# Kernel tuning notes

Measured on AMD Instinct MI355X. Metric: run time of the kernel, lower is better.

Reference implementation:

```python
import jax, jax.numpy as jnp
import numpy as np

B, S, D = 4, 4096, 1024
H = 16
HD = D // H  # 64
EPS = 1e-6


def setup_inputs() -> dict:
    key = jax.random.key(0)
    ks = jax.random.split(key, 7)
    scale = 1.0 / np.sqrt(D)
    return {
        "hidden_states": jax.random.normal(ks[0], (B, S, D), dtype=jnp.float32),
        "Wq": jax.random.normal(ks[1], (D, D), dtype=jnp.float32) * scale,
        "bq": jax.random.normal(ks[2], (D,), dtype=jnp.float32) * 0.02,
        "Wk": jax.random.normal(ks[3], (D, D), dtype=jnp.float32) * scale,
        "bk": jax.random.normal(ks[4], (D,), dtype=jnp.float32) * 0.02,
        "Wv": jax.random.normal(ks[5], (D, D), dtype=jnp.float32) * scale,
        "bv": jax.random.normal(ks[6], (D,), dtype=jnp.float32) * 0.02,
    }


def _heads(x):
    # [B,S,D] -> [B,H,S,HD]
    return x.reshape(B, S, H, HD).transpose(0, 2, 1, 3)


def reference(hidden_states, Wq, bq, Wk, bk, Wv, bv):
    q = _heads(hidden_states @ Wq + bq)
    k = _heads(hidden_states @ Wk + bk)
    v = _heads(hidden_states @ Wv + bv)
    # elu+1 feature maps
    q_feat = jax.nn.elu(q) + 1.0
    k_feat = jax.nn.elu(k) + 1.0
    # kv: [B,H,HD,HD]; k_sum: [B,H,HD]
    kv = jnp.einsum("bhsd,bhse->bhde", k_feat, v)
    k_sum = k_feat.sum(axis=2)
    numerator = jnp.einsum("bhsd,bhde->bhse", q_feat, kv)
    denominator = jnp.einsum("bhsd,bhd->bhs", q_feat, k_sum)
    denominator = jnp.maximum(denominator, EPS)
    out = numerator / denominator[..., None]  # [B,H,S,HD]
    return out.transpose(0, 2, 1, 3).reshape(B, S, D)
```

## Files before the change

kernel.cpp:

```cpp
#include <hip/hip_runtime.h>
#include <math.h>

#define BB 4
#define SS 4096
#define DD 1024
#define HH 16
#define HDD 64
#define MM (BB*SS)
#define EPSV 1e-6f

typedef __bf16 bf16x8 __attribute__((ext_vector_type(8)));
typedef float  f32x4  __attribute__((ext_vector_type(4)));
typedef unsigned short ushort_t;

__device__ __forceinline__ float bf2f(unsigned int u16) {
    return __uint_as_float(u16 << 16);
}
__device__ __forceinline__ unsigned short f2bf(float f) {
    unsigned int x = __float_as_uint(f);
    unsigned int r = x + 0x7fffu + ((x >> 16) & 1u);
    return (unsigned short)(r >> 16);
}

#define GLDS16(g, l) __builtin_amdgcn_global_load_lds( \
    (const __attribute__((address_space(1))) void*)(g), \
    (__attribute__((address_space(3))) void*)(l), 16, 0, 0)

__global__ __launch_bounds__(256) void cvt_hs(const float* __restrict__ in,
                                              ushort_t* __restrict__ out) {
    size_t i = ((size_t)blockIdx.x * 256 + threadIdx.x) * 8;
    float4 f0 = *reinterpret_cast<const float4*>(&in[i]);
    float4 f1 = *reinterpret_cast<const float4*>(&in[i + 4]);
    uint4 u;
    u.x = (unsigned)f2bf(f0.x) | ((unsigned)f2bf(f0.y) << 16);
    u.y = (unsigned)f2bf(f0.z) | ((unsigned)f2bf(f0.w) << 16);
    u.z = (unsigned)f2bf(f1.x) | ((unsigned)f2bf(f1.y) << 16);
    u.w = (unsigned)f2bf(f1.z) | ((unsigned)f2bf(f1.w) << 16);
    *reinterpret_cast<uint4*>(&out[i]) = u;
}

__global__ __launch_bounds__(256) void cvt_w(const float* __restrict__ Wq,
                                             const float* __restrict__ Wk,
                                             const float* __restrict__ Wv,
                                             ushort_t* __restrict__ wt) {
    const int z = blockIdx.z;
    const float* __restrict__ W = (z == 0) ? Wq : (z == 1) ? Wk : Wv;
    const int k0 = blockIdx.x * 64;
    const int n0 = blockIdx.y * 64;
    __shared__ float tile[64][65];
    const int t = threadIdx.x;
    {
        const int kk = t >> 2;
        const int c0 = (t & 3) * 16;
#pragma unroll
        for (int c = 0; c < 4; c++) {
            float4 v = *reinterpret_cast<const float4*>(&W[(size_t)(k0 + kk) * DD + n0 + c0 + c * 4]);
            tile[kk][c0 + c * 4 + 0] = v.x;
            tile[kk][c0 + c * 4 + 1] = v.y;
            tile[kk][c0 + c * 4 + 2] = v.z;
            tile[kk][c0 + c * 4 + 3] = v.w;
        }
    }
    __syncthreads();
    const int n = t >> 2;
    const int kc = t & 3;
    unsigned short tmp[16];
#pragma unroll
    for (int jj = 0; jj < 16; jj++) tmp[jj] = f2bf(tile[kc * 16 + jj][n]);
    uint4 u0, u1;
    u0.x = tmp[0] | (tmp[1] << 16);  u0.y = tmp[2] | (tmp[3] << 16);
    u0.z = tmp[4] | (tmp[5] << 16);  u0.w = tmp[6] | (tmp[7] << 16);
    u1.x = tmp[8] | (tmp[9] << 16);  u1.y = tmp[10] | (tmp[11] << 16);
    u1.z = tmp[12] | (tmp[13] << 16); u1.w = tmp[14] | (tmp[15] << 16);
    ushort_t* dst = &wt[((size_t)z << 20) + (size_t)(n0 + n) * DD + k0 + kc * 16];
    *reinterpret_cast<uint4*>(dst) = u0;
    *reinterpret_cast<uint4*>(dst + 8) = u1;
}

__global__ __launch_bounds__(256) void qkv_gemm_bf16(
    const ushort_t* __restrict__ A,
    const ushort_t* __restrict__ Bt,
    const float* __restrict__ bq, const float* __restrict__ bk, const float* __restrict__ bv,
    ushort_t* __restrict__ qf, ushort_t* __restrict__ kt, ushort_t* __restrict__ vt)
{
    const int id  = blockIdx.x;
    const int swz = (id & 7) * 384 + (id >> 3);
    const int z   = swz >> 10;
    const int rem = swz & 1023;
    const int m0  = (rem >> 3) * 128;
    const int n0  = (rem & 7) * 128;

    const ushort_t* __restrict__ Bz = Bt + ((size_t)z << 20);
    const float* __restrict__ bias  = (z == 0) ? bq : (z == 1) ? bk : bv;

    __shared__ ushort_t As[128 * 32];
    __shared__ ushort_t Bs[128 * 32];

    const int tid = threadIdx.x;
    const int lane = tid & 63;
    const int w  = tid >> 6;
    const int wr = w >> 1;
    const int wc = w & 1;

    f32x4 acc[4][4];
#pragma unroll
    for (int i = 0; i < 4; i++)
#pragma unroll
        for (int j = 0; j < 4; j++) acc[i][j] = (f32x4){0.f, 0.f, 0.f, 0.f};

    const int lrow = lane >> 2;
    const int lkc  = (lane & 3) * 8;
    const int fr = lane & 15;
    const int fk = (lane >> 4) * 8;

    for (int k0 = 0; k0 < DD; k0 += 32) {
        __syncthreads();
#pragma unroll
        for (int si = 0; si < 2; si++) {
            const int seg = w * 2 + si;
            GLDS16(&A [(size_t)(m0 + seg * 16 + lrow) * DD + k0 + lkc], &As[seg * 512]);
            GLDS16(&Bz[(size_t)(n0 + seg * 16 + lrow) * DD + k0 + lkc], &Bs[seg * 512]);
        }
        __syncthreads();
        bf16x8 a[4], b[4];
#pragma unroll
        for (int i = 0; i < 4; i++)
            a[i] = *reinterpret_cast<const bf16x8*>(&As[(wr * 64 + i * 16 + fr) * 32 + fk]);
#pragma unroll
        for (int j = 0; j < 4; j++)
            b[j] = *reinterpret_cast<const bf16x8*>(&Bs[(wc * 64 + j * 16 + fr) * 32 + fk]);
#pragma unroll
        for (int i = 0; i < 4; i++)
#pragma unroll
            for (int j = 0; j < 4; j++)
                acc[i][j] = __builtin_amdgcn_mfma_f32_16x16x32_bf16(a[i], b[j], acc[i][j], 0, 0, 0);
    }

    const int fq = lane >> 4;
    float bias4[4];
#pragma unroll
    for (int j = 0; j < 4; j++) bias4[j] = bias[n0 + wc * 64 + j * 16 + fr];

    if (z == 0) {
#pragma unroll
        for (int i = 0; i < 4; i++) {
#pragma unroll
            for (int r = 0; r < 4; r++) {
                const int m = m0 + wr * 64 + i * 16 + fq * 4 + r;
                const int bI = m >> 12;
                const int s  = m & 4095;
#pragma unroll
                for (int j = 0; j < 4; j++) {
                    const int n = n0 + wc * 64 + j * 16 + fr;
                    const int h = n >> 6, e = n & 63;
                    float c = acc[i][j][r] + bias4[j];
                    c = (c > 0.f) ? (c + 1.f) : __expf(c);
                    qf[((size_t)(bI * HH + h) * SS + s) * HDD + e] = f2bf(c);
                }
            }
        }
    } else {
        ushort_t* __restrict__ outt = (z == 1) ? kt : vt;
        const bool isk = (z == 1);
#pragma unroll
        for (int i = 0; i < 4; i++) {
            const int m = m0 + wr * 64 + i * 16 + fq * 4;
            const int bI = m >> 12;
            const int s  = m & 4095;
#pragma unroll
            for (int j = 0; j < 4; j++) {
                const int n = n0 + wc * 64 + j * 16 + fr;
                const int h = n >> 6, e = n & 63;
                ushort4 u;
                float c0 = acc[i][j][0] + bias4[j];
                float c1 = acc[i][j][1] + bias4[j];
                float c2 = acc[i][j][2] + bias4[j];
                float c3 = acc[i][j][3] + bias4[j];
                if (isk) {
                    c0 = (c0 > 0.f) ? (c0 + 1.f) : __expf(c0);
                    c1 = (c1 > 0.f) ? (c1 + 1.f) : __expf(c1);
                    c2 = (c2 > 0.f) ? (c2 + 1.f) : __expf(c2);
                    c3 = (c3 > 0.f) ? (c3 + 1.f) : __expf(c3);
                }
                u.x = f2bf(c0); u.y = f2bf(c1); u.z = f2bf(c2); u.w = f2bf(c3);
                *reinterpret_cast<ushort4*>(
                    &outt[((size_t)((bI * HH + h) * HDD + e)) * SS + s]) = u;
            }
        }
    }
}

__global__ __launch_bounds__(256) void kv_mfma(
    const ushort_t* __restrict__ kt, const ushort_t* __restrict__ vt,
    float* __restrict__ kv_part, float* __restrict__ ksum_part)
{
    const int bh = blockIdx.x;
    const int c  = blockIdx.y;
    const int tid = threadIdx.x;
    const int lane = tid & 63;
    const int w = tid >> 6;
    const int fr = lane & 15;
    const int fq = lane >> 4;

    const size_t base = (size_t)bh * HDD * SS;
    const int s0 = c * 512;

    bf16x8 ones;
#pragma unroll
    for (int x = 0; x < 8; x++) ones[x] = (__bf16)1.0f;

    f32x4 acc[4], ks[4];
#pragma unroll
    for (int i = 0; i < 4; i++) { acc[i] = (f32x4){0,0,0,0}; ks[i] = (f32x4){0,0,0,0}; }

#pragma unroll
    for (int ksi = 0; ksi < 16; ksi++) {
        const int sc = s0 + ksi * 32 + fq * 8;
        bf16x8 a[4];
#pragma unroll
        for (int i = 0; i < 4; i++)
            a[i] = *reinterpret_cast<const bf16x8*>(&kt[base + (size_t)(i * 16 + fr) * SS + sc]);
        bf16x8 b = *reinterpret_cast<const bf16x8*>(&vt[base + (size_t)(w * 16 + fr) * SS + sc]);
#pragma unroll
        for (int i = 0; i < 4; i++) {
            acc[i] = __builtin_amdgcn_mfma_f32_16x16x32_bf16(a[i], b, acc[i], 0, 0, 0);
            ks[i]  = __builtin_amdgcn_mfma_f32_16x16x32_bf16(a[i], ones, ks[i], 0, 0, 0);
        }
    }

    float* kp = kv_part + ((size_t)(bh * 8 + c) << 12);
#pragma unroll
    for (int i = 0; i < 4; i++)
#pragma unroll
        for (int r = 0; r < 4; r++)
            kp[(i * 16 + fq * 4 + r) * 64 + (w * 16 + fr)] = acc[i][r];
    if (w == 0 && fr == 0) {
        float* ksp = ksum_part + (size_t)(bh * 8 + c) * 64;
#pragma unroll
        for (int i = 0; i < 4; i++)
#pragma unroll
            for (int r = 0; r < 4; r++)
                ksp[i * 16 + fq * 4 + r] = ks[i][r];
    }
}

__global__ __launch_bounds__(256) void kv_finalize(
    const float* __restrict__ kv_part, const float* __restrict__ ksum_part,
    ushort_t* __restrict__ kvh, ushort_t* __restrict__ kvl, float* __restrict__ ksum)
{
    const int bh = blockIdx.x;
    const int tid = threadIdx.x;
    __shared__ float lin[4096];

    const float* kp = kv_part + ((size_t)(bh * 8) << 12);
    float s[16];
#pragma unroll
    for (int x = 0; x < 16; x++) s[x] = 0.f;
#pragma unroll
    for (int cc = 0; cc < 8; cc++) {
#pragma unroll
        for (int g = 0; g < 4; g++) {
            float4 v = *reinterpret_cast<const float4*>(&kp[((size_t)cc << 12) + tid * 16 + g * 4]);
            s[g * 4 + 0] += v.x; s[g * 4 + 1] += v.y;
            s[g * 4 + 2] += v.z; s[g * 4 + 3] += v.w;
        }
    }
#pragma unroll
    for (int g = 0; g < 4; g++) {
        float4 v = make_float4(s[g * 4], s[g * 4 + 1], s[g * 4 + 2], s[g * 4 + 3]);
        *reinterpret_cast<float4*>(&lin[tid * 16 + g * 4]) = v;
    }
    if (tid < 64) {
        float t = 0.f;
#pragma unroll
        for (int cc = 0; cc < 8; cc++) t += ksum_part[(size_t)(bh * 8 + cc) * 64 + tid];
        ksum[bh * 64 + tid] = t;
    }
    __syncthreads();

    const int e  = tid >> 2;
    const int db = tid & 3;
    ushort_t hi[16], lo[16];
#pragma unroll
    for (int dd = 0; dd < 16; dd++) {
        float v = lin[(db * 16 + dd) * 64 + e];
        hi[dd] = f2bf(v);
        lo[dd] = f2bf(v - bf2f(hi[dd]));
    }
    ushort_t* ph = &kvh[(size_t)bh * 4096 + e * 64 + db * 16];
    ushort_t* pl = &kvl[(size_t)bh * 4096 + e * 64 + db * 16];
#pragma unroll
    for (int g = 0; g < 2; g++) {
        uint4 uh, ul;
        uh.x = hi[g*8+0] | (hi[g*8+1] << 16); uh.y = hi[g*8+2] | (hi[g*8+3] << 16);
        uh.z = hi[g*8+4] | (hi[g*8+5] << 16); uh.w = hi[g*8+6] | (hi[g*8+7] << 16);
        ul.x = lo[g*8+0] | (lo[g*8+1] << 16); ul.y = lo[g*8+2] | (lo[g*8+3] << 16);
        ul.z = lo[g*8+4] | (lo[g*8+5] << 16); ul.w = lo[g*8+6] | (lo[g*8+7] << 16);
        *reinterpret_cast<uint4*>(ph + g * 8) = uh;
        *reinterpret_cast<uint4*>(pl + g * 8) = ul;
    }
}

__global__ __launch_bounds__(256) void out_mfma(
    const ushort_t* __restrict__ qf, const ushort_t* __restrict__ kvh,
    const ushort_t* __restrict__ kvl, const float* __restrict__ ksum,
    float* __restrict__ outp)
{
    const int bh = blockIdx.x;
    const int s0 = blockIdx.y * 64;
    const int bI = bh >> 4, h = bh & 15;
    const int tid = threadIdx.x;

    __shared__ float kss[64];
    __shared__ float denp[64][4];
    __shared__ float dens[64];

    if (tid < 64) kss[tid] = ksum[bh * 64 + tid];
    __syncthreads();

    {
        const int sr = tid >> 2, dq = tid & 3;
        const ushort_t* qp = qf + (size_t)bh * SS * HDD + (size_t)(s0 + sr) * HDD + dq * 16;
        uint4 u0 = *reinterpret_cast<const uint4*>(qp);
        uint4 u1 = *reinterpret_cast<const uint4*>(qp + 8);
        const float* kb = &kss[dq * 16];
        float p = 0.f;
        p += bf2f(u0.x & 0xffff) * kb[0];  p += bf2f(u0.x >> 16) * kb[1];
        p += bf2f(u0.y & 0xffff) * kb[2];  p += bf2f(u0.y >> 16) * kb[3];
        p += bf2f(u0.z & 0xffff) * kb[4];  p += bf2f(u0.z >> 16) * kb[5];
        p += bf2f(u0.w & 0xffff) * kb[6];  p += bf2f(u0.w >> 16) * kb[7];
        p += bf2f(u1.x & 0xffff) * kb[8];  p += bf2f(u1.x >> 16) * kb[9];
        p += bf2f(u1.y & 0xffff) * kb[10]; p += bf2f(u1.y >> 16) * kb[11];
        p += bf2f(u1.z & 0xffff) * kb[12]; p += bf2f(u1.z >> 16) * kb[13];
        p += bf2f(u1.w & 0xffff) * kb[14]; p += bf2f(u1.w >> 16) * kb[15];
        denp[sr][dq] = p;
    }
    __syncthreads();
    if (tid < 64)
        dens[tid] = fmaxf(denp[tid][0] + denp[tid][1] + denp[tid][2] + denp[tid][3], EPSV);
    __syncthreads();

    const int lane = tid & 63, w = tid >> 6;
    const int fr = lane & 15, fq = lane >> 4;

    const ushort_t* qb = qf + (size_t)bh * SS * HDD + (size_t)(s0 + w * 16 + fr) * HDD + fq * 8;
    bf16x8 a0 = *reinterpret_cast<const bf16x8*>(qb);
    bf16x8 a1 = *reinterpret_cast<const bf16x8*>(qb + 32);

    f32x4 acc[4];
#pragma unroll
    for (int j = 0; j < 4; j++) acc[j] = (f32x4){0.f, 0.f, 0.f, 0.f};

    const ushort_t* hb = kvh + ((size_t)bh << 12) + (size_t)fr * HDD + fq * 8;
    const ushort_t* lb = kvl + ((size_t)bh << 12) + (size_t)fr * HDD + fq * 8;
#pragma unroll
    for (int j = 0; j < 4; j++) {
        const ushort_t* hj = hb + (size_t)j * 16 * HDD;
        const ushort_t* lj = lb + (size_t)j * 16 * HDD;
        bf16x8 bh0 = *reinterpret_cast<const bf16x8*>(hj);
        bf16x8 bh1 = *reinterpret_cast<const bf16x8*>(hj + 32);
        bf16x8 bl0 = *reinterpret_cast<const bf16x8*>(lj);
        bf16x8 bl1 = *reinterpret_cast<const bf16x8*>(lj + 32);
        acc[j] = __builtin_amdgcn_mfma_f32_16x16x32_bf16(a0, bh0, acc[j], 0, 0, 0);
        acc[j] = __builtin_amdgcn_mfma_f32_16x16x32_bf16(a1, bh1, acc[j], 0, 0, 0);
        acc[j] = __builtin_amdgcn_mfma_f32_16x16x32_bf16(a0, bl0, acc[j], 0, 0, 0);
        acc[j] = __builtin_amdgcn_mfma_f32_16x16x32_bf16(a1, bl1, acc[j], 0, 0, 0);
    }

#pragma unroll
    for (int r = 0; r < 4; r++) {
        const int srow = w * 16 + fq * 4 + r;
        const float inv = 1.0f / dens[srow];
        float* ob = outp + ((size_t)(bI * SS + s0 + srow)) * DD + h * HDD;
#pragma unroll
        for (int j = 0; j < 4; j++)
            ob[j * 16 + fr] = acc[j][r] * inv;
    }
}

extern "C" void kernel_launch(void* const* d_in, const int* in_sizes, int n_in,
                              void* d_out, int out_size, void* d_ws, size_t ws_size,
                              hipStream_t stream) {
    const float* hs = (const float*)d_in[0];
    const float* Wq = (const float*)d_in[1];
    const float* bq = (const float*)d_in[2];
    const float* Wk = (const float*)d_in[3];
    const float* bk = (const float*)d_in[4];
    const float* Wv = (const float*)d_in[5];
    const float* bv = (const float*)d_in[6];
    float* outp = (float*)d_out;

    ushort_t* hs_bf    = (ushort_t*)d_ws;
    ushort_t* wt_bf    = hs_bf + (size_t)MM * DD;
    ushort_t* qf       = wt_bf + ((size_t)3 << 20);
    float*    kv_part  = (float*)(qf + (size_t)MM * DD);
    float*    ksum_prt = kv_part + ((size_t)64 * 8 << 12);
    ushort_t* kvh      = (ushort_t*)(ksum_prt + 64 * 8 * 64);
    ushort_t* kvl      = kvh + (size_t)64 * 4096;
    float*    ksum     = (float*)(kvl + (size_t)64 * 4096);
    ushort_t* kt = (ushort_t*)d_out;
    ushort_t* vt = kt + (size_t)MM * DD;

    hipLaunchKernelGGL(cvt_hs, dim3((MM * DD) / (256 * 8)), dim3(256), 0, stream, hs, hs_bf);
    hipLaunchKernelGGL(cvt_w, dim3(16, 16, 3), dim3(256), 0, stream, Wq, Wk, Wv, wt_bf);

    hipLaunchKernelGGL(qkv_gemm_bf16, dim3(3072), dim3(256), 0, stream,
                       hs_bf, wt_bf, bq, bk, bv, qf, kt, vt);

    hipLaunchKernelGGL(kv_mfma, dim3(64, 8), dim3(256), 0, stream, kt, vt, kv_part, ksum_prt);
    hipLaunchKernelGGL(kv_finalize, dim3(64), dim3(256), 0, stream,
                       kv_part, ksum_prt, kvh, kvl, ksum);
    hipLaunchKernelGGL(out_mfma, dim3(64, 64), dim3(256), 0, stream,
                       qf, kvh, kvl, ksum, outp);
}
```

Before: 342.1 us.

## Stage QKV epilogue through LDS and fuse kv finalize into output kernel

The GEMM epilogue now writes bias+feature-mapped tiles into a padded shared buffer and then emits coalesced 16-byte row stores for q, k^T and v^T, replacing scattered 2- and 8-byte global stores. The kv_finalize kernel is removed: each output block reduces the 8 partial kv/ksum slices itself, does the hi/lo bf16 split in registers, and computes the denominator with MFMA instead of a scalar dot product. This drops a launch and an intermediate round trip, but every one of the 4096 output blocks now repeats the partial reduction, reading about 128KB of kv_part each, and the GEMM gets a larger LDS footprint.

Measured after the change: 337.2 us. About the same (-1.4%).

```diff
diff --git a/kernel.cpp b/kernel.cpp
--- a/kernel.cpp
+++ b/kernel.cpp
@@ -8,10 +8,14 @@
 #define HDD 64
 #define MM (BB*SS)
 #define EPSV 1e-6f
+#define CS 136
 
 typedef __bf16 bf16x8 __attribute__((ext_vector_type(8)));
 typedef float  f32x4  __attribute__((ext_vector_type(4)));
+typedef unsigned short u16x8 __attribute__((ext_vector_type(8)));
 typedef unsigned short ushort_t;
+
+union BFU { u16x8 u; bf16x8 b; };
 
 __device__ __forceinline__ float bf2f(unsigned int u16) {
     return __uint_as_float(u16 << 16);
@@ -93,8 +97,9 @@
     const ushort_t* __restrict__ Bz = Bt + ((size_t)z << 20);
     const float* __restrict__ bias  = (z == 0) ? bq : (z == 1) ? bk : bv;
 
-    __shared__ ushort_t As[128 * 32];
-    __shared__ ushort_t Bs[128 * 32];
+    __shared__ ushort_t smem[128 * CS];
+    ushort_t* As = smem;
+    ushort_t* Bs = smem + 4096;
 
     const int tid = threadIdx.x;
     const int lane = tid & 63;
@@ -136,6 +141,8 @@
                 acc[i][j] = __builtin_amdgcn_mfma_f32_16x16x32_bf16(a[i], b[j], acc[i][j], 0, 0, 0);
     }
 
+    __syncthreads();
+
     const int fq = lane >> 4;
     float bias4[4];
 #pragma unroll
@@ -143,50 +150,57 @@
 
     if (z == 0) {
 #pragma unroll
-        for (int i = 0; i < 4; i++) {
+        for (int i = 0; i < 4; i++)
 #pragma unroll
             for (int r = 0; r < 4; r++) {
-                const int m = m0 + wr * 64 + i * 16 + fq * 4 + r;
-                const int bI = m >> 12;
-                const int s  = m & 4095;
+                const int row = wr * 64 + i * 16 + fq * 4 + r;
 #pragma unroll
                 for (int j = 0; j < 4; j++) {
-                    const int n = n0 + wc * 64 + j * 16 + fr;
-                    const int h = n >> 6, e = n & 63;
+                    const int col = wc * 64 + j * 16 + fr;
                     float c = acc[i][j][r] + bias4[j];
                     c = (c > 0.f) ? (c + 1.f) : __expf(c);
-                    qf[((size_t)(bI * HH + h) * SS + s) * HDD + e] = f2bf(c);
+                    smem[row * CS + col] = f2bf(c);
                 }
             }
-        }
+    } else {
+        const bool isk = (z == 1);
+#pragma unroll
+        for (int i = 0; i < 4; i++)
+#pragma unroll
+            for (int r = 0; r < 4; r++) {
+                const int row = wr * 64 + i * 16 + fq * 4 + r;
+#pragma unroll
+                for (int j = 0; j < 4; j++) {
+                    const int col = wc * 64 + j * 16 + fr;
+                    float c = acc[i][j][r] + bias4[j];
+                    if (isk) c = (c > 0.f) ? (c + 1.f) : __expf(c);
+                    smem[col * CS + row] = f2bf(c);
+                }
+            }
+    }
+    __syncthreads();
+
+    const int rowh = tid & 127;
+    const int half = tid >> 7;
+    const int bI = m0 >> 12;
+    const ushort_t* src = &smem[rowh * CS + half * 64];
+
+    if (z == 0) {
+        const int s = (m0 & 4095) + rowh;
+        const int h = (n0 >> 6) + half;
+        ushort_t* dst = &qf[((size_t)(bI * HH + h) * SS + s) * HDD];
+#pragma unroll
+        for (int g = 0; g < 8; g++)
+            *reinterpret_cast<uint4*>(dst + g * 8) = *reinterpret_cast<const uint4*>(src + g * 8);
     } else {
         ushort_t* __restrict__ outt = (z == 1) ? kt : vt;
-        const bool isk = (z == 1);
-#pragma unroll
-        for (int i = 0; i < 4; i++) {
-            const int m = m0 + wr * 64 + i * 16 + fq * 4;
-            const int bI = m >> 12;
-            const int s  = m & 4095;
-#pragma unroll
-            for (int j = 0; j < 4; j++) {
-                const int n = n0 + wc * 64 + j * 16 + fr;
-                const int h = n >> 6, e = n & 63;
-                ushort4 u;
-                float c0 = acc[i][j][0] + bias4[j];
-                float c1 = acc[i][j][1] + bias4[j];
-                float c2 = acc[i][j][2] + bias4[j];
-                float c3 = acc[i][j][3] + bias4[j];
-                if (isk) {
-                    c0 = (c0 > 0.f) ? (c0 + 1.f) : __expf(c0);
-                    c1 = (c1 > 0.f) ? (c1 + 1.f) : __expf(c1);
-                    c2 = (c2 > 0.f) ? (c2 + 1.f) : __expf(c2);
-                    c3 = (c3 > 0.f) ? (c3 + 1.f) : __expf(c3);
-                }
-                u.x = f2bf(c0); u.y = f2bf(c1); u.z = f2bf(c2); u.w = f2bf(c3);
-                *reinterpret_cast<ushort4*>(
-                    &outt[((size_t)((bI * HH + h) * HDD + e)) * SS + s]) = u;
-            }
-        }
+        const int n = n0 + rowh;
+        const int h = n >> 6, e = n & 63;
+        const int sb = (m0 & 4095) + half * 64;
+        ushort_t* dst = &outt[((size_t)((bI * HH + h) * HDD + e)) * SS + sb];
+#pragma unroll
+        for (int g = 0; g < 8; g++)
+            *reinterpret_cast<uint4*>(dst + g * 8) = *reinterpret_cast<const uint4*>(src + g * 8);
     }
 }
 
@@ -244,137 +258,98 @@
     }
 }
 
-__global__ __launch_bounds__(256) void kv_finalize(
-    const float* __restrict__ kv_part, const float* __restrict__ ksum_part,
-    ushort_t* __restrict__ kvh, ushort_t* __restrict__ kvl, float* __restrict__ ksum)
-{
-    const int bh = blockIdx.x;
-    const int tid = threadIdx.x;
-    __shared__ float lin[4096];
-
-    const float* kp = kv_part + ((size_t)(bh * 8) << 12);
-    float s[16];
-#pragma unroll
-    for (int x = 0; x < 16; x++) s[x] = 0.f;
-#pragma unroll
-    for (int cc = 0; cc < 8; cc++) {
-#pragma unroll
-        for (int g = 0; g < 4; g++) {
-            float4 v = *reinterpret_cast<const float4*>(&kp[((size_t)cc << 12) + tid * 16 + g * 4]);
-            s[g * 4 + 0] += v.x; s[g * 4 + 1] += v.y;
-            s[g * 4 + 2] += v.z; s[g * 4 + 3] += v.w;
-        }
-    }
-#pragma unroll
-    for (int g = 0; g < 4; g++) {
-        float4 v = make_float4(s[g * 4], s[g * 4 + 1], s[g * 4 + 2], s[g * 4 + 3]);
-        *reinterpret_cast<float4*>(&lin[tid * 16 + g * 4]) = v;
-    }
-    if (tid < 64) {
-        float t = 0.f;
-#pragma unroll
-        for (int cc = 0; cc < 8; cc++) t += ksum_part[(size_t)(bh * 8 + cc) * 64 + tid];
-        ksum[bh * 64 + tid] = t;
-    }
-    __syncthreads();
-
-    const int e  = tid >> 2;
-    const int db = tid & 3;
-    ushort_t hi[16], lo[16];
-#pragma unroll
-    for (int dd = 0; dd < 16; dd++) {
-        float v = lin[(db * 16 + dd) * 64 + e];
-        hi[dd] = f2bf(v);
-        lo[dd] = f2bf(v - bf2f(hi[dd]));
-    }
-    ushort_t* ph = &kvh[(size_t)bh * 4096 + e * 64 + db * 16];
-    ushort_t* pl = &kvl[(size_t)bh * 4096 + e * 64 + db * 16];
-#pragma unroll
-    for (int g = 0; g < 2; g++) {
-        uint4 uh, ul;
-        uh.x = hi[g*8+0] | (hi[g*8+1] << 16); uh.y = hi[g*8+2] | (hi[g*8+3] << 16);
-        uh.z = hi[g*8+4] | (hi[g*8+5] << 16); uh.w = hi[g*8+6] | (hi[g*8+7] << 16);
-        ul.x = lo[g*8+0] | (lo[g*8+1] << 16); ul.y = lo[g*8+2] | (lo[g*8+3] << 16);
-        ul.z = lo[g*8+4] | (lo[g*8+5] << 16); ul.w = lo[g*8+6] | (lo[g*8+7] << 16);
-        *reinterpret_cast<uint4*>(ph + g * 8) = uh;
-        *reinterpret_cast<uint4*>(pl + g * 8) = ul;
-    }
-}
-
-__global__ __launch_bounds__(256) void out_mfma(
-    const ushort_t* __restrict__ qf, const ushort_t* __restrict__ kvh,
-    const ushort_t* __restrict__ kvl, const float* __restrict__ ksum,
-    float* __restrict__ outp)
+__global__ __launch_bounds__(256) void out_fused(
+    const ushort_t* __restrict__ qf, const float* __restrict__ kv_part,
+    const float* __restrict__ ksum_part, float* __restrict__ outp)
 {
     const int bh = blockIdx.x;
     const int s0 = blockIdx.y * 64;
     const int bI = bh >> 4, h = bh & 15;
     const int tid = threadIdx.x;
 
+    __shared__ float kvf[64 * 65];
     __shared__ float kss[64];
-    __shared__ float denp[64][4];
-    __shared__ float dens[64];
-
-    if (tid < 64) kss[tid] = ksum[bh * 64 + tid];
-    __syncthreads();
 
     {
-        const int sr = tid >> 2, dq = tid & 3;
-        const ushort_t* qp = qf + (size_t)bh * SS * HDD + (size_t)(s0 + sr) * HDD + dq * 16;
-        uint4 u0 = *reinterpret_cast<const uint4*>(qp);
-        uint4 u1 = *reinterpret_cast<const uint4*>(qp + 8);
-        const float* kb = &kss[dq * 16];
-        float p = 0.f;
-        p += bf2f(u0.x & 0xffff) * kb[0];  p += bf2f(u0.x >> 16) * kb[1];
-        p += bf2f(u0.y & 0xffff) * kb[2];  p += bf2f(u0.y >> 16) * kb[3];
-        p += bf2f(u0.z & 0xffff) * kb[4];  p += bf2f(u0.z >> 16) * kb[5];
-        p += bf2f(u0.w & 0xffff) * kb[6];  p += bf2f(u0.w >> 16) * kb[7];
-        p += bf2f(u1.x & 0xffff) * kb[8];  p += bf2f(u1.x >> 16) * kb[9];
-        p += bf2f(u1.y & 0xffff) * kb[10]; p += bf2f(u1.y >> 16) * kb[11];
-        p += bf2f(u1.z & 0xffff) * kb[12]; p += bf2f(u1.z >> 16) * kb[13];
-        p += bf2f(u1.w & 0xffff) * kb[14]; p += bf2f(u1.w >> 16) * kb[15];
-        denp[sr][dq] = p;
-    }
-    __syncthreads();
-    if (tid < 64)
-        dens[tid] = fmaxf(denp[tid][0] + denp[tid][1] + denp[tid][2] + denp[tid][3], EPSV);
+        const int d  = tid >> 2;
+        const int eg = (tid & 3) * 16;
+        float s16[16];
+#pragma unroll
+        for (int x = 0; x < 16; x++) s16[x] = 0.f;
+#pragma unroll
+        for (int c = 0; c < 8; c++) {
+            const float* kp = kv_part + (((size_t)(bh * 8 + c)) << 12) + d * 64 + eg;
+#pragma unroll
+            for (int g = 0; g < 4; g++) {
+                float4 v = *reinterpret_cast<const float4*>(&kp[g * 4]);
+                s16[g * 4 + 0] += v.x; s16[g * 4 + 1] += v.y;
+                s16[g * 4 + 2] += v.z; s16[g * 4 + 3] += v.w;
+            }
+        }
+#pragma unroll
+        for (int x = 0; x < 16; x++) kvf[d * 65 + eg + x] = s16[x];
+        if (tid < 64) {
+            float t = 0.f;
+#pragma unroll
+            for (int c = 0; c < 8; c++) t += ksum_part[(size_t)(bh * 8 + c) * 64 + tid];
+            kss[tid] = t;
+        }
+    }
     __syncthreads();
 
     const int lane = tid & 63, w = tid >> 6;
     const int fr = lane & 15, fq = lane >> 4;
 
-    const ushort_t* qb = qf + (size_t)bh * SS * HDD + (size_t)(s0 + w * 16 + fr) * HDD + fq * 8;
+    const ushort_t* qb = qf + ((size_t)bh * SS + s0 + w * 16 + fr) * HDD + fq * 8;
     bf16x8 a0 = *reinterpret_cast<const bf16x8*>(qb);
     bf16x8 a1 = *reinterpret_cast<const bf16x8*>(qb + 32);
 
-    f32x4 acc[4];
-#pragma unroll
-    for (int j = 0; j < 4; j++) acc[j] = (f32x4){0.f, 0.f, 0.f, 0.f};
-
-    const ushort_t* hb = kvh + ((size_t)bh << 12) + (size_t)fr * HDD + fq * 8;
-    const ushort_t* lb = kvl + ((size_t)bh << 12) + (size_t)fr * HDD + fq * 8;
+    BFU kh0, kh1, kl0, kl1;
+#pragma unroll
+    for (int t = 0; t < 8; t++) {
+        float v0 = kss[fq * 8 + t];
+        float v1 = kss[32 + fq * 8 + t];
+        unsigned short h0 = f2bf(v0), h1 = f2bf(v1);
+        kh0.u[t] = h0; kl0.u[t] = f2bf(v0 - bf2f(h0));
+        kh1.u[t] = h1; kl1.u[t] = f2bf(v1 - bf2f(h1));
+    }
+
+    f32x4 accn[4], accd;
+#pragma unroll
+    for (int j = 0; j < 4; j++) accn[j] = (f32x4){0.f, 0.f, 0.f, 0.f};
+    accd = (f32x4){0.f, 0.f, 0.f, 0.f};
+
+    accd = __builtin_amdgcn_mfma_f32_16x16x32_bf16(a0, kh0.b, accd, 0, 0, 0);
+    accd = __builtin_amdgcn_mfma_f32_16x16x32_bf16(a1, kh1.b, accd, 0, 0, 0);
+    accd = __builtin_amdgcn_mfma_f32_16x16x32_bf16(a0, kl0.b, accd, 0, 0, 0);
+    accd = __builtin_amdgcn_mfma_f32_16x16x32_bf16(a1, kl1.b, accd, 0, 0, 0);
+
 #pragma unroll
     for (int j = 0; j < 4; j++) {
-        const ushort_t* hj = hb + (size_t)j * 16 * HDD;
-        const ushort_t* lj = lb + (size_t)j * 16 * HDD;
-        bf16x8 bh0 = *reinterpret_cast<const bf16x8*>(hj);
-        bf16x8 bh1 = *reinterpret_cast<const bf16x8*>(hj + 32);
-        bf16x8 bl0 = *reinterpret_cast<const bf16x8*>(lj);
-        bf16x8 bl1 = *reinterpret_cast<const bf16x8*>(lj + 32);
-        acc[j] = __builtin_amdgcn_mfma_f32_16x16x32_bf16(a0, bh0, acc[j], 0, 0, 0);
-        acc[j] = __builtin_amdgcn_mfma_f32_16x16x32_bf16(a1, bh1, acc[j], 0, 0, 0);
-        acc[j] = __builtin_amdgcn_mfma_f32_16x16x32_bf16(a0, bl0, acc[j], 0, 0, 0);
-        acc[j] = __builtin_amdgcn_mfma_f32_16x16x32_bf16(a1, bl1, acc[j], 0, 0, 0);
+        const int e = j * 16 + fr;
+        BFU bh0, bh1, bl0, bl1;
+#pragma unroll
+        for (int t = 0; t < 8; t++) {
+            float v0 = kvf[(fq * 8 + t) * 65 + e];
+            float v1 = kvf[(32 + fq * 8 + t) * 65 + e];
+            unsigned short h0 = f2bf(v0), h1 = f2bf(v1);
+            bh0.u[t] = h0; bl0.u[t] = f2bf(v0 - bf2f(h0));
+            bh1.u[t] = h1; bl1.u[t] = f2bf(v1 - bf2f(h1));
+        }
+        accn[j] = __builtin_amdgcn_mfma_f32_16x16x32_bf16(a0, bh0.b, accn[j], 0, 0, 0);
+        accn[j] = __builtin_amdgcn_mfma_f32_16x16x32_bf16(a1, bh1.b, accn[j], 0, 0, 0);
+        accn[j] = __builtin_amdgcn_mfma_f32_16x16x32_bf16(a0, bl0.b, accn[j], 0, 0, 0);
+        accn[j] = __builtin_amdgcn_mfma_f32_16x16x32_bf16(a1, bl1.b, accn[j], 0, 0, 0);
     }
 
 #pragma unroll
     for (int r = 0; r < 4; r++) {
         const int srow = w * 16 + fq * 4 + r;
-        const float inv = 1.0f / dens[srow];
+        const float inv = 1.0f / fmaxf(accd[r], EPSV);
         float* ob = outp + ((size_t)(bI * SS + s0 + srow)) * DD + h * HDD;
 #pragma unroll
         for (int j = 0; j < 4; j++)
-            ob[j * 16 + fr] = acc[j][r] * inv;
+            ob[j * 16 + fr] = accn[j][r] * inv;
     }
 }
 
@@ -395,9 +370,6 @@
     ushort_t* qf       = wt_bf + ((size_t)3 << 20);
     float*    kv_part  = (float*)(qf + (size_t)MM * DD);
     float*    ksum_prt = kv_part + ((size_t)64 * 8 << 12);
-    ushort_t* kvh      = (ushort_t*)(ksum_prt + 64 * 8 * 64);
-    ushort_t* kvl      = kvh + (size_t)64 * 4096;
-    float*    ksum     = (float*)(kvl + (size_t)64 * 4096);
     ushort_t* kt = (ushort_t*)d_out;
     ushort_t* vt = kt + (size_t)MM * DD;
 
@@ -408,8 +380,6 @@
                        hs_bf, wt_bf, bq, bk, bv, qf, kt, vt);
 
     hipLaunchKernelGGL(kv_mfma, dim3(64, 8), dim3(256), 0, stream, kt, vt, kv_part, ksum_prt);
-    hipLaunchKernelGGL(kv_finalize, dim3(64), dim3(256), 0, stream,
-                       kv_part, ksum_prt, kvh, kvl, ksum);
-    hipLaunchKernelGGL(out_mfma, dim3(64, 64), dim3(256), 0, stream,
-                       qf, kvh, kvl, ksum, outp);
-}
+    hipLaunchKernelGGL(out_fused, dim3(64, 64), dim3(256), 0, stream,
+                       qf, kv_part, ksum_prt, outp);
+}
```
